# Kernel tuning notes

Hardware: AMD Instinct MI355X
Metric: run time of the kernel (lower is better)

Reference implementation:

```python
import jax, jax.numpy as jnp
import numpy as np


def setup_inputs() -> dict:
    key = jax.random.key(0)
    k1, k2, k3, k4 = jax.random.split(key, 4)
    B, D, N, M = 4, 256, 4096, 4096
    return {
        "src": jax.random.normal(k1, (B, 3, N), dtype=jnp.float32),
        "tgt": jax.random.normal(k2, (B, 3, M), dtype=jnp.float32),
        "src_emb": jax.random.normal(k3, (B, D, N), dtype=jnp.float32),
        "tgt_emb": jax.random.normal(k4, (B, D, M), dtype=jnp.float32),
    }


def reference(src, tgt, src_emb, tgt_emb):
    # pairwise_distance[b,n,m] = -||src_emb[:,n] - tgt_emb[:,m]||^2
    # decomposed as -xx + 2*inner - yy (inner below is -2*dot, as in torch code)
    inner = -2.0 * jnp.einsum("bdn,bdm->bnm", src_emb, tgt_emb)       # [B,N,M]
    xx = jnp.sum(src_emb ** 2, axis=1)[:, :, None]                     # [B,N,1]
    yy = jnp.sum(tgt_emb ** 2, axis=1)[:, None, :]                     # [B,1,M]
    pairwise_distance = -xx - inner - yy                               # [B,N,M]
    scores = jax.nn.softmax(pairwise_distance, axis=2)                 # softmax over tgt points
    # src_corr[b,c,n] = sum_m tgt[b,c,m] * scores[b,n,m]
    src_corr = jnp.einsum("bcm,bnm->bcn", tgt, scores)                 # [B,3,N]
    return src_corr
```

## Files before the change

kernel.cpp:

```cpp
#include <hip/hip_runtime.h>

#define NBATCH 4
#define DDIM   256
#define NN     4096
#define MM     4096
#define NCHUNK 8
#define MCHUNK 512
#define MTILE  64
#define LOG2E  1.44269504088896340736f

using half8   = __attribute__((ext_vector_type(8))) _Float16;
using floatx4 = __attribute__((ext_vector_type(4))) float;


__global__ __launch_bounds__(256) void k_prep(const float* __restrict__ src_emb,
                                              const float* __restrict__ tgt_emb,
                                              const float* __restrict__ tgt,
                                              _Float16* __restrict__ Qf,
                                              _Float16* __restrict__ Kf,
                                              float* __restrict__ yyS,
                                              float4* __restrict__ Vt) {
    __shared__ float psum[4][64];
    int i = blockIdx.x;
    int xcd = i & 7, j = i >> 3;
    int b = xcd >> 1, nhalf = xcd & 1;
    int tensor = j & 1, sub = j >> 1;
    int n0 = nhalf * 2048 + sub * 64;
    const float* in = tensor ? tgt_emb : src_emb;
    _Float16* outp  = tensor ? Kf : Qf;
    const float scale = tensor ? 1.0f : 2.0f * LOG2E;
    int t = threadIdx.x, w = t >> 6, ln = t & 63;
    const float* ib = in + (size_t)b * DDIM * NN + n0 + ln;
    _Float16* ob = outp + (size_t)b * NN * 32 * 8;
    int blk = (n0 + ln) >> 4, l15 = ln & 15;
    float ss = 0.f;
#pragma unroll
    for (int h = 0; h < 2; h++) {
        int ds = w + h * 4;
#pragma unroll
        for (int oct = 0; oct < 4; oct++) {
            half8 v;
#pragma unroll
            for (int k = 0; k < 8; k++) {
                float f = ib[(size_t)(ds * 32 + oct * 8 + k) * NN];
                ss = fmaf(f, f, ss);
                v[k] = (_Float16)(f * scale);
            }
            *(half8*)(ob + ((((size_t)blk * 8 + ds) * 4 + oct) * 16 + l15) * 8) = v;
        }
    }
    if (tensor) psum[w][ln] = ss;
    __syncthreads();
    if (tensor) {
        if (t < 64) {
            float s = psum[0][t] + psum[1][t] + psum[2][t] + psum[3][t];
            yyS[b * MM + n0 + t] = s * (-LOG2E);
        } else if (t < 128) {
            int m = n0 + (t - 64);
            const float* tp = tgt + (size_t)b * 3 * MM + m;
            Vt[(size_t)b * MM + m] = make_float4(tp[0], tp[MM], tp[2 * MM], 1.0f);
        }
    }
}

__global__ __launch_bounds__(256, 2) void k_flash(const _Float16* __restrict__ Qf,
                                                  const _Float16* __restrict__ Kf,
                                                  const float* __restrict__ yyS,
                                                  const float4* __restrict__ Vt,
                                                  float4* __restrict__ Opart,
                                                  float* __restrict__ Mpart) {
    __shared__ __align__(16) _Float16 Kt[2][MTILE * DDIM];
    __shared__ floatx4 vtt[MCHUNK];
    __shared__ floatx4 yyt[MCHUNK / 4];

    int i = blockIdx.x, t = threadIdx.x;
    int xcd = i & 7, j = i >> 3;
    int b = xcd >> 1, nhalf = xcd & 1;
    int chunk = j & 7, ntile = nhalf * 8 + (j >> 3);

    int wave = t >> 6, lane = t & 63, quad = lane >> 4, l15 = lane & 15;
    int m0 = chunk * MCHUNK;
    int mblk0 = m0 >> 4;

    const char* kfb = (const char*)(Kf + (size_t)b * NN * DDIM);
    auto stage = [&](int mt) {
        const char* gb = kfb + (size_t)(mblk0 + mt * 4) * 8192 + wave * 8192;
        char* lb = (char*)&Kt[mt & 1][0] + wave * 8192;
#pragma unroll
        for (int it = 0; it < 8; it++) {
            __builtin_amdgcn_global_load_lds(
                (const __attribute__((address_space(1))) uint32_t*)(const void*)
                    (gb + it * 1024 + lane * 16),
                (__attribute__((address_space(3))) uint32_t*)(void*)
                    (lb + it * 1024),
                16, 0, 0);
        }
    };

    stage(0);

    {
        const float4* vb = Vt + (size_t)b * MM + m0;
        for (int r = t; r < MCHUNK; r += 256) {
            float4 g = vb[r];
            vtt[r] = (floatx4){g.x, g.y, g.z, g.w};
        }
        const floatx4* yb = (const floatx4*)(yyS + (size_t)b * MM + m0);
        if (t < MCHUNK / 4) yyt[t] = yb[t];
    }

    int nblk0 = ntile * 16 + wave * 4;
    const half8* qp = (const half8*)Qf + (size_t)b * NN * 32;
    half8 qf[4][8];
#pragma unroll
    for (int nb = 0; nb < 4; nb++)
#pragma unroll
        for (int ds = 0; ds < 8; ds++)
            qf[nb][ds] = qp[(((size_t)(nblk0 + nb) * 8 + ds) * 4 + quad) * 16 + l15];

    const floatx4 z4 = {0.f, 0.f, 0.f, 0.f};
    floatx4 o[4] = {z4, z4, z4, z4};
    float mr[4];
#pragma unroll
    for (int nb = 0; nb < 4; nb++) mr[nb] = -__builtin_inff();

    for (int mt = 0; mt < MCHUNK / MTILE; mt++) {
        __syncthreads();
        if (mt + 1 < MCHUNK / MTILE) stage(mt + 1);

        const char* Kb = (const char*)&Kt[mt & 1][0];
#pragma unroll
        for (int mb = 0; mb < 4; mb++) {
            const char* rb = Kb + mb * 8192 + lane * 16;
            half8 a[8];
#pragma unroll
            for (int ds = 0; ds < 8; ds++) a[ds] = *(const half8*)(rb + ds * 1024);

            floatx4 acc[4] = {z4, z4, z4, z4};
#pragma unroll
            for (int ds = 0; ds < 8; ds++)
#pragma unroll
                for (int nb = 0; nb < 4; nb++)
                    acc[nb] = __builtin_amdgcn_mfma_f32_16x16x32_f16(a[ds], qf[nb][ds], acc[nb], 0, 0, 0);

            floatx4 yv = yyt[mt * 16 + mb * 4 + quad];
            floatx4 vr[4];
#pragma unroll
            for (int r = 0; r < 4; r++) vr[r] = vtt[mt * MTILE + mb * 16 + quad * 4 + r];
#pragma unroll
            for (int nb = 0; nb < 4; nb++) {
                acc[nb] = acc[nb] + yv;
                float tm = fmaxf(fmaxf(acc[nb][0], acc[nb][1]), fmaxf(acc[nb][2], acc[nb][3]));
                float mn = fmaxf(mr[nb], tm);
                float al = __builtin_amdgcn_exp2f(mr[nb] - mn);
                mr[nb] = mn;
                o[nb] = o[nb] * al;
#pragma unroll
                for (int r = 0; r < 4; r++) {
                    float p = __builtin_amdgcn_exp2f(acc[nb][r] - mn);
                    o[nb] = o[nb] + p * vr[r];
                }
            }
        }
    }

#pragma unroll
    for (int nb = 0; nb < 4; nb++) {
        float mq = mr[nb];
        float ma = fmaxf(mq, __shfl_xor(mq, 16, 64));
        ma = fmaxf(ma, __shfl_xor(ma, 32, 64));
        float wgt = __builtin_amdgcn_exp2f(mq - ma);
        floatx4 ow = o[nb] * wgt;
#pragma unroll
        for (int c = 0; c < 4; c++) {
            float v = ow[c];
            v += __shfl_xor(v, 16, 64);
            v += __shfl_xor(v, 32, 64);
            ow[c] = v;
        }
        if (quad == 0) {
            int n = (nblk0 + nb) * 16 + l15;
            size_t idx = (size_t)(chunk * NBATCH + b) * NN + n;
            Opart[idx] = make_float4(ow[0], ow[1], ow[2], ow[3]);
            Mpart[idx] = ma;
        }
    }
}

__global__ __launch_bounds__(128) void k_combine(const float4* __restrict__ Opart,
                                                 const float* __restrict__ Mpart,
                                                 float* __restrict__ out) {
    int idx = blockIdx.x * 128 + threadIdx.x;
    int b = idx >> 12, n = idx & (NN - 1);
    float mstar = -__builtin_inff();
#pragma unroll
    for (int j = 0; j < NCHUNK; j++)
        mstar = fmaxf(mstar, Mpart[(size_t)(j * NBATCH + b) * NN + n]);
    float o0 = 0.f, o1 = 0.f, o2 = 0.f, l = 0.f;
#pragma unroll
    for (int j = 0; j < NCHUNK; j++) {
        size_t id = (size_t)(j * NBATCH + b) * NN + n;
        float w = __builtin_amdgcn_exp2f(Mpart[id] - mstar);
        float4 P = Opart[id];
        o0 = fmaf(w, P.x, o0); o1 = fmaf(w, P.y, o1);
        o2 = fmaf(w, P.z, o2); l  = fmaf(w, P.w, l);
    }
    out[(size_t)(b * 3 + 0) * NN + n] = o0 / l;
    out[(size_t)(b * 3 + 1) * NN + n] = o1 / l;
    out[(size_t)(b * 3 + 2) * NN + n] = o2 / l;
}

extern "C" void kernel_launch(void* const* d_in, const int* in_sizes, int n_in,
                              void* d_out, int out_size, void* d_ws, size_t ws_size,
                              hipStream_t stream) {
    const float* tgt     = (const float*)d_in[1];
    const float* src_emb = (const float*)d_in[2];
    const float* tgt_emb = (const float*)d_in[3];
    float* out = (float*)d_out;

    char* ws = (char*)d_ws;
    _Float16* Qf  = (_Float16*)(ws);
    _Float16* Kf  = (_Float16*)(ws + 8388608);
    float*    yyS = (float*)   (ws + 16777216);
    float4*   Vt  = (float4*)  (ws + 16842752);
    float4*   Op  = (float4*)  (ws + 17104896);
    float*    Mp  = (float*)   (ws + 19202048);

    hipLaunchKernelGGL(k_prep,    dim3(512), dim3(256), 0, stream,
                       src_emb, tgt_emb, tgt, Qf, Kf, yyS, Vt);
    hipLaunchKernelGGL(k_flash,   dim3(512), dim3(256), 0, stream, Qf, Kf, yyS, Vt, Op, Mp);
    hipLaunchKernelGGL(k_combine, dim3(128), dim3(128), 0, stream, Op, Mp, out);
}
```

Measured before the change: 125.9 us.

## Shrink flash tiles for higher occupancy, vectorize prep, fold yy bias into V

The flash kernel now uses 32-wide M tiles and 2 N-blocks per wave, launching 1024 blocks with a 4-blocks-per-CU launch bound to raise occupancy and cut register pressure. The yy bias is folded into the V table's fourth component, which removes the separate yy shared-memory table, and the row-sum now uses a plain add instead of a multiply by one. The prep kernel loads float4 vectors, handles 256 columns per block split across two D-groups, and writes yy both into Vt.w and into yyS. The trade-off is less Q reuse per K load from shared memory and more blocks re-reading K.

```diff
diff --git a/kernel.cpp b/kernel.cpp
--- a/kernel.cpp
+++ b/kernel.cpp
@@ -6,7 +6,7 @@
 #define MM     4096
 #define NCHUNK 8
 #define MCHUNK 512
-#define MTILE  64
+#define MTILE  32
 #define LOG2E  1.44269504088896340736f
 
 using half8   = __attribute__((ext_vector_type(8))) _Float16;
@@ -20,50 +20,62 @@
                                               _Float16* __restrict__ Kf,
                                               float* __restrict__ yyS,
                                               float4* __restrict__ Vt) {
-    __shared__ float psum[4][64];
+    __shared__ float psum[4][256];
     int i = blockIdx.x;
-    int xcd = i & 7, j = i >> 3;
-    int b = xcd >> 1, nhalf = xcd & 1;
-    int tensor = j & 1, sub = j >> 1;
-    int n0 = nhalf * 2048 + sub * 64;
+    int tensor = i & 1, b = (i >> 1) & 3, dg = (i >> 3) & 1, ng = i >> 4;
+    int t = threadIdx.x, w = t >> 6, lane = t & 63;
+    int ds = dg * 4 + w;
     const float* in = tensor ? tgt_emb : src_emb;
     _Float16* outp  = tensor ? Kf : Qf;
     const float scale = tensor ? 1.0f : 2.0f * LOG2E;
-    int t = threadIdx.x, w = t >> 6, ln = t & 63;
-    const float* ib = in + (size_t)b * DDIM * NN + n0 + ln;
-    _Float16* ob = outp + (size_t)b * NN * 32 * 8;
-    int blk = (n0 + ln) >> 4, l15 = ln & 15;
-    float ss = 0.f;
-#pragma unroll
-    for (int h = 0; h < 2; h++) {
-        int ds = w + h * 4;
-#pragma unroll
-        for (int oct = 0; oct < 4; oct++) {
-            half8 v;
-#pragma unroll
-            for (int k = 0; k < 8; k++) {
-                float f = ib[(size_t)(ds * 32 + oct * 8 + k) * NN];
-                ss = fmaf(f, f, ss);
-                v[k] = (_Float16)(f * scale);
-            }
-            *(half8*)(ob + ((((size_t)blk * 8 + ds) * 4 + oct) * 16 + l15) * 8) = v;
-        }
-    }
-    if (tensor) psum[w][ln] = ss;
-    __syncthreads();
+
+    const float* ibase = in + ((size_t)b * DDIM + ds * 32) * NN + ng * 256;
+    float4 f[4][8];
+#pragma unroll
+    for (int oct = 0; oct < 4; oct++)
+#pragma unroll
+        for (int k = 0; k < 8; k++)
+            f[oct][k] = ((const float4*)(ibase + (size_t)(oct * 8 + k) * NN))[lane];
+
+    half8* ob = (half8*)(outp + (size_t)b * NN * DDIM);
+    int n0 = ng * 256 + lane * 4;
+    float ss0 = 0.f, ss1 = 0.f, ss2 = 0.f, ss3 = 0.f;
+#pragma unroll
+    for (int oct = 0; oct < 4; oct++) {
+        half8 v[4];
+#pragma unroll
+        for (int k = 0; k < 8; k++) {
+            float4 g = f[oct][k];
+            ss0 = fmaf(g.x, g.x, ss0);  ss1 = fmaf(g.y, g.y, ss1);
+            ss2 = fmaf(g.z, g.z, ss2);  ss3 = fmaf(g.w, g.w, ss3);
+            v[0][k] = (_Float16)(g.x * scale);
+            v[1][k] = (_Float16)(g.y * scale);
+            v[2][k] = (_Float16)(g.z * scale);
+            v[3][k] = (_Float16)(g.w * scale);
+        }
+#pragma unroll
+        for (int j = 0; j < 4; j++) {
+            int n = n0 + j;
+            ob[(((size_t)(n >> 4) * 8 + ds) * 4 + oct) * 16 + (n & 15)] = v[j];
+        }
+    }
     if (tensor) {
-        if (t < 64) {
-            float s = psum[0][t] + psum[1][t] + psum[2][t] + psum[3][t];
-            yyS[b * MM + n0 + t] = s * (-LOG2E);
-        } else if (t < 128) {
-            int m = n0 + (t - 64);
+        psum[w][lane * 4 + 0] = ss0;  psum[w][lane * 4 + 1] = ss1;
+        psum[w][lane * 4 + 2] = ss2;  psum[w][lane * 4 + 3] = ss3;
+        __syncthreads();
+        int m = ng * 256 + t;
+        float s = (psum[0][t] + psum[1][t]) + (psum[2][t] + psum[3][t]);
+        s *= -LOG2E;
+        if (dg == 0) {
             const float* tp = tgt + (size_t)b * 3 * MM + m;
-            Vt[(size_t)b * MM + m] = make_float4(tp[0], tp[MM], tp[2 * MM], 1.0f);
-        }
-    }
-}
-
-__global__ __launch_bounds__(256, 2) void k_flash(const _Float16* __restrict__ Qf,
+            Vt[(size_t)b * MM + m] = make_float4(tp[0], tp[MM], tp[2 * MM], s);
+        } else {
+            yyS[(size_t)b * MM + m] = s;
+        }
+    }
+}
+
+__global__ __launch_bounds__(256, 4) void k_flash(const _Float16* __restrict__ Qf,
                                                   const _Float16* __restrict__ Kf,
                                                   const float* __restrict__ yyS,
                                                   const float4* __restrict__ Vt,
@@ -71,12 +83,11 @@
                                                   float* __restrict__ Mpart) {
     __shared__ __align__(16) _Float16 Kt[2][MTILE * DDIM];
     __shared__ floatx4 vtt[MCHUNK];
-    __shared__ floatx4 yyt[MCHUNK / 4];
 
     int i = blockIdx.x, t = threadIdx.x;
     int xcd = i & 7, j = i >> 3;
     int b = xcd >> 1, nhalf = xcd & 1;
-    int chunk = j & 7, ntile = nhalf * 8 + (j >> 3);
+    int chunk = j & 7, ntile = nhalf * 16 + (j >> 3);
 
     int wave = t >> 6, lane = t & 63, quad = lane >> 4, l15 = lane & 15;
     int m0 = chunk * MCHUNK;
@@ -84,10 +95,10 @@
 
     const char* kfb = (const char*)(Kf + (size_t)b * NN * DDIM);
     auto stage = [&](int mt) {
-        const char* gb = kfb + (size_t)(mblk0 + mt * 4) * 8192 + wave * 8192;
-        char* lb = (char*)&Kt[mt & 1][0] + wave * 8192;
-#pragma unroll
-        for (int it = 0; it < 8; it++) {
+        const char* gb = kfb + (size_t)(mblk0 + mt * 2) * 8192 + wave * 4096;
+        char* lb = (char*)&Kt[mt & 1][0] + wave * 4096;
+#pragma unroll
+        for (int it = 0; it < 4; it++) {
             __builtin_amdgcn_global_load_lds(
                 (const __attribute__((address_space(1))) uint32_t*)(const void*)
                     (gb + it * 1024 + lane * 16),
@@ -101,28 +112,25 @@
 
     {
         const float4* vb = Vt + (size_t)b * MM + m0;
+        const float* yb = yyS + (size_t)b * MM + m0;
         for (int r = t; r < MCHUNK; r += 256) {
             float4 g = vb[r];
-            vtt[r] = (floatx4){g.x, g.y, g.z, g.w};
-        }
-        const floatx4* yb = (const floatx4*)(yyS + (size_t)b * MM + m0);
-        if (t < MCHUNK / 4) yyt[t] = yb[t];
-    }
-
-    int nblk0 = ntile * 16 + wave * 4;
+            vtt[r] = (floatx4){g.x, g.y, g.z, g.w + yb[r]};
+        }
+    }
+
+    int nblk0 = ntile * 8 + wave * 2;
     const half8* qp = (const half8*)Qf + (size_t)b * NN * 32;
-    half8 qf[4][8];
-#pragma unroll
-    for (int nb = 0; nb < 4; nb++)
+    half8 qf[2][8];
+#pragma unroll
+    for (int nb = 0; nb < 2; nb++)
 #pragma unroll
         for (int ds = 0; ds < 8; ds++)
             qf[nb][ds] = qp[(((size_t)(nblk0 + nb) * 8 + ds) * 4 + quad) * 16 + l15];
 
     const floatx4 z4 = {0.f, 0.f, 0.f, 0.f};
-    floatx4 o[4] = {z4, z4, z4, z4};
-    float mr[4];
-#pragma unroll
-    for (int nb = 0; nb < 4; nb++) mr[nb] = -__builtin_inff();
+    floatx4 o[2] = {z4, z4};
+    float mr[2] = {-__builtin_inff(), -__builtin_inff()};
 
     for (int mt = 0; mt < MCHUNK / MTILE; mt++) {
         __syncthreads();
@@ -130,42 +138,43 @@
 
         const char* Kb = (const char*)&Kt[mt & 1][0];
 #pragma unroll
-        for (int mb = 0; mb < 4; mb++) {
+        for (int mb = 0; mb < 2; mb++) {
             const char* rb = Kb + mb * 8192 + lane * 16;
-            half8 a[8];
-#pragma unroll
-            for (int ds = 0; ds < 8; ds++) a[ds] = *(const half8*)(rb + ds * 1024);
-
-            floatx4 acc[4] = {z4, z4, z4, z4};
-#pragma unroll
-            for (int ds = 0; ds < 8; ds++)
-#pragma unroll
-                for (int nb = 0; nb < 4; nb++)
-                    acc[nb] = __builtin_amdgcn_mfma_f32_16x16x32_f16(a[ds], qf[nb][ds], acc[nb], 0, 0, 0);
-
-            floatx4 yv = yyt[mt * 16 + mb * 4 + quad];
+            floatx4 acc[2] = {z4, z4};
+#pragma unroll
+            for (int ds = 0; ds < 8; ds++) {
+                half8 a = *(const half8*)(rb + ds * 1024);
+                acc[0] = __builtin_amdgcn_mfma_f32_16x16x32_f16(a, qf[0][ds], acc[0], 0, 0, 0);
+                acc[1] = __builtin_amdgcn_mfma_f32_16x16x32_f16(a, qf[1][ds], acc[1], 0, 0, 0);
+            }
+
             floatx4 vr[4];
 #pragma unroll
             for (int r = 0; r < 4; r++) vr[r] = vtt[mt * MTILE + mb * 16 + quad * 4 + r];
 #pragma unroll
-            for (int nb = 0; nb < 4; nb++) {
-                acc[nb] = acc[nb] + yv;
-                float tm = fmaxf(fmaxf(acc[nb][0], acc[nb][1]), fmaxf(acc[nb][2], acc[nb][3]));
+            for (int nb = 0; nb < 2; nb++) {
+                float s[4];
+#pragma unroll
+                for (int r = 0; r < 4; r++) s[r] = acc[nb][r] + vr[r][3];
+                float tm = fmaxf(fmaxf(s[0], s[1]), fmaxf(s[2], s[3]));
                 float mn = fmaxf(mr[nb], tm);
                 float al = __builtin_amdgcn_exp2f(mr[nb] - mn);
                 mr[nb] = mn;
                 o[nb] = o[nb] * al;
 #pragma unroll
                 for (int r = 0; r < 4; r++) {
-                    float p = __builtin_amdgcn_exp2f(acc[nb][r] - mn);
-                    o[nb] = o[nb] + p * vr[r];
+                    float p = __builtin_amdgcn_exp2f(s[r] - mn);
+                    o[nb][0] = fmaf(p, vr[r][0], o[nb][0]);
+                    o[nb][1] = fmaf(p, vr[r][1], o[nb][1]);
+                    o[nb][2] = fmaf(p, vr[r][2], o[nb][2]);
+                    o[nb][3] += p;
                 }
             }
         }
     }
 
 #pragma unroll
-    for (int nb = 0; nb < 4; nb++) {
+    for (int nb = 0; nb < 2; nb++) {
         float mq = mr[nb];
         float ma = fmaxf(mq, __shfl_xor(mq, 16, 64));
         ma = fmaxf(ma, __shfl_xor(ma, 32, 64));
@@ -226,8 +235,8 @@
     float4*   Op  = (float4*)  (ws + 17104896);
     float*    Mp  = (float*)   (ws + 19202048);
 
-    hipLaunchKernelGGL(k_prep,    dim3(512), dim3(256), 0, stream,
+    hipLaunchKernelGGL(k_prep,    dim3(256),  dim3(256), 0, stream,
                        src_emb, tgt_emb, tgt, Qf, Kf, yyS, Vt);
-    hipLaunchKernelGGL(k_flash,   dim3(512), dim3(256), 0, stream, Qf, Kf, yyS, Vt, Op, Mp);
-    hipLaunchKernelGGL(k_combine, dim3(128), dim3(128), 0, stream, Op, Mp, out);
-}
+    hipLaunchKernelGGL(k_flash,   dim3(1024), dim3(256), 0, stream, Qf, Kf, yyS, Vt, Op, Mp);
+    hipLaunchKernelGGL(k_combine, dim3(128),  dim3(128), 0, stream, Op, Mp, out);
+}
```

Measured after the change: 132.4 us. 1.05x slower.
